# Kernel optimization log

Measured on AMD Instinct MI355X. Metric: run time of the kernel, lower is better.

The kernel has to match this reference:

```python
import jax, jax.numpy as jnp
import numpy as np

N_NODES = 50000
N_EDGES = 800000
N_PAIRS = 200000
IN_DIM = 128
HID = 64
OUT_DIM = 1


def _gat_layer(x, W, a_l, a_r, src, dst, n_nodes):
    # Single-head GAT (DGL-style): z = xW; attention logits from learned
    # left/right vectors; softmax over incoming edges of each dst node.
    z = x @ W                                   # [N, H]
    el = z @ a_l                                # [N]
    er = z @ a_r                                # [N]
    e = jax.nn.leaky_relu(el[src] + er[dst], 0.2)   # [E]
    emax = jax.ops.segment_max(e, dst, num_segments=n_nodes)  # [N]
    ex = jnp.exp(e - emax[dst])                 # [E], stable softmax numerator
    denom = jax.ops.segment_sum(ex, dst, num_segments=n_nodes)  # [N]
    msg = ex[:, None] * z[src]                  # [E, H]
    agg = jax.ops.segment_sum(msg, dst, num_segments=n_nodes)   # [N, H]
    return agg / jnp.maximum(denom, 1e-9)[:, None]


def setup_inputs() -> dict:
    key = jax.random.key(0)
    ks = jax.random.split(key, 10)
    feat = jax.random.normal(ks[0], (N_NODES, IN_DIM), dtype=jnp.float32)
    src = jax.random.randint(ks[1], (N_EDGES,), 0, N_NODES, dtype=jnp.int32)
    dst = jax.random.randint(ks[2], (N_EDGES,), 0, N_NODES, dtype=jnp.int32)
    # query pairs: take existing edges so the has_edges_between mask is true
    pair_src = src[:N_PAIRS]
    pair_dst = dst[:N_PAIRS]
    s1 = 1.0 / np.sqrt(IN_DIM)
    s2 = 1.0 / np.sqrt(HID)
    W1 = jax.random.normal(ks[3], (IN_DIM, HID), dtype=jnp.float32) * s1
    al1 = jax.random.normal(ks[4], (HID,), dtype=jnp.float32) * s2
    ar1 = jax.random.normal(ks[5], (HID,), dtype=jnp.float32) * s2
    W2 = jax.random.normal(ks[6], (HID, HID), dtype=jnp.float32) * s2
    al2 = jax.random.normal(ks[7], (HID,), dtype=jnp.float32) * s2
    ar2 = jax.random.normal(ks[8], (HID,), dtype=jnp.float32) * s2
    Wc = jax.random.normal(ks[9], (2 * HID, OUT_DIM), dtype=jnp.float32) * s2
    bc = jnp.zeros((OUT_DIM,), dtype=jnp.float32)
    return {"feat": feat, "W1": W1, "al1": al1, "ar1": ar1,
            "W2": W2, "al2": al2, "ar2": ar2, "Wc": Wc, "bc": bc,
            "src": src, "dst": dst, "pair_src": pair_src, "pair_dst": pair_dst}


def reference(feat, W1, al1, ar1, W2, al2, ar2, Wc, bc, src, dst, pair_src, pair_dst):
    src = src.astype(jnp.int32)
    dst = dst.astype(jnp.int32)
    # two hetero GAT layers (single ntype -> mean aggregate is identity) + ReLU
    h = jax.nn.relu(_gat_layer(feat, W1, al1, ar1, src, dst, N_NODES))
    h = jax.nn.relu(_gat_layer(h, W2, al2, ar2, src, dst, N_NODES))
    # has_edges_between(pair_src, pair_dst): membership test via sorted edge keys
    ekeys = src.astype(jnp.int64) * N_NODES + dst.astype(jnp.int64)
    skeys = jnp.sort(ekeys)
    pkeys = pair_src.astype(jnp.int64) * N_NODES + pair_dst.astype(jnp.int64)
    idx = jnp.clip(jnp.searchsorted(skeys, pkeys), 0, N_EDGES - 1)
    mask = (skeys[idx] == pkeys)                 # [P] bool
    # gather endpoint embeddings, concat, classify, sigmoid; invalid rows -> 0
    hs = h[pair_src]                             # [P, H]
    hd = h[pair_dst]                             # [P, H]
    h_pair = jnp.concatenate([hs, hd], axis=1)   # [P, 2H]
    out = jax.nn.sigmoid(h_pair @ Wc + bc)       # [P, OUT]
    return out * mask[:, None].astype(out.dtype)
```

## Files before the change

### kernel.cpp

```cpp
#include <hip/hip_runtime.h>
#include <cstdint>

#define N_NODES 50000
#define N_EDGES 800000
#define N_PAIRS 200000
#define IN_DIM 128
#define HID 64
#define N_WAVES_GEMM (N_NODES / 16)
#define NB1 196
#define CHUNK ((N_EDGES + NB1 - 1) / NB1)
#define MHIST (NB1 * NB1)
#define SBG ((MHIST + 255) / 256)
#define MB_GEMM ((N_WAVES_GEMM + 3) / 4)
#define NODE_BLOCKS ((N_NODES + 3) / 4)
#define MEMBER_BLOCKS (N_PAIRS / 32)

typedef __attribute__((ext_vector_type(8))) short bf16x8;
typedef __attribute__((ext_vector_type(4))) float f32x4;

__device__ __forceinline__ unsigned short bf16_rne(float f) {
    unsigned u = __float_as_uint(f);
    unsigned t = u + 0x7FFFu + ((u >> 16) & 1u);
    return (unsigned short)(t >> 16);
}
__device__ __forceinline__ void bf2f(unsigned u, float& a, float& b) {
    a = __uint_as_float(u << 16);
    b = __uint_as_float(u & 0xFFFF0000u);
}

__global__ __launch_bounds__(256) void hist_prep(
    const int* __restrict__ dst, int* __restrict__ histHi,
    const float* __restrict__ W1, const float* __restrict__ W2,
    unsigned short* __restrict__ w1hi, unsigned short* __restrict__ w1lo,
    unsigned short* __restrict__ w2hi, unsigned short* __restrict__ w2lo)
{
    const int t = threadIdx.x, b = blockIdx.x;
    if (b < NB1) {
        __shared__ int hist[256];
        hist[t] = 0; __syncthreads();
        const int beg = b * CHUNK, end = min(beg + CHUNK, N_EDGES);
        for (int e = beg + t; e < end; e += 256) atomicAdd(&hist[dst[e] >> 8], 1);
        __syncthreads();
        if (t < NB1) histHi[t * NB1 + b] = hist[t];
    } else {
        int tid = (b - NB1) * 256 + t;
        if (tid < 8192) {
            int jj = tid & 7, lane = (tid >> 3) & 63, tt = (tid >> 9) & 3, ks = tid >> 11;
            int k = ks * 32 + (lane >> 4) * 8 + jj;
            int n = tt * 16 + (lane & 15);
            float f = W1[k * HID + n];
            unsigned short hi = bf16_rne(f);
            float fhi = __uint_as_float(((unsigned)hi) << 16);
            w1hi[tid] = hi;
            w1lo[tid] = bf16_rne(f - fhi);
        }
        if (tid < 4096) {
            int jj = tid & 7, lane = (tid >> 3) & 63, tt = (tid >> 9) & 3, ks = tid >> 11;
            int k = ks * 32 + (lane >> 4) * 8 + jj;
            int n = tt * 16 + (lane & 15);
            float f = W2[k * HID + n];
            unsigned short hi = bf16_rne(f);
            float fhi = __uint_as_float(((unsigned)hi) << 16);
            w2hi[tid] = hi;
            w2lo[tid] = bf16_rne(f - fhi);
        }
    }
}

__global__ __launch_bounds__(256) void scan1g(
    int* __restrict__ histHi, int* __restrict__ bsums)
{
    __shared__ int sh[256];
    const int t = threadIdx.x;
    const int i = blockIdx.x * 256 + t;
    int v = (i < MHIST) ? histHi[i] : 0;
    sh[t] = v; __syncthreads();
    #pragma unroll
    for (int off = 1; off < 256; off <<= 1) {
        int x = sh[t];
        int a = (t >= off) ? sh[t - off] : 0;
        __syncthreads();
        sh[t] = x + a;
        __syncthreads();
    }
    if (i < MHIST) histHi[i] = sh[t] - v;
    if (t == 255) bsums[blockIdx.x] = sh[255];
}

__device__ __forceinline__ void scan_bsums(const int* __restrict__ bsums,
                                           int* sh, int* exb, int t)
{
    int v = (t < SBG) ? bsums[t] : 0;
    sh[t] = v; __syncthreads();
    #pragma unroll
    for (int off = 1; off < 256; off <<= 1) {
        int x = sh[t];
        int a = (t >= off) ? sh[t - off] : 0;
        __syncthreads();
        sh[t] = x + a;
        __syncthreads();
    }
    exb[t] = sh[t] - v;
    __syncthreads();
}

__device__ __forceinline__ void gemm1_body(
    int wave, int lane,
    const float* __restrict__ x,
    const unsigned short* __restrict__ whi, const unsigned short* __restrict__ wlo,
    const float* __restrict__ al, const float* __restrict__ ar,
    unsigned short* __restrict__ z, float* __restrict__ el, float* __restrict__ er)
{
    const int i0 = wave * 16;
    const int m = lane & 15, quad = lane >> 4;
    f32x4 acc[4] = {{0.f,0.f,0.f,0.f},{0.f,0.f,0.f,0.f},{0.f,0.f,0.f,0.f},{0.f,0.f,0.f,0.f}};
    const float* xrow = x + (size_t)(i0 + m) * IN_DIM;

    #pragma unroll 1
    for (int ks = 0; ks < 4; ++ks) {
        const float4 xv0 = *(const float4*)&xrow[ks * 32 + quad * 8];
        const float4 xv1 = *(const float4*)&xrow[ks * 32 + quad * 8 + 4];
        float xs[8] = {xv0.x, xv0.y, xv0.z, xv0.w, xv1.x, xv1.y, xv1.z, xv1.w};
        bf16x8 ahi, alo;
        #pragma unroll
        for (int jj = 0; jj < 8; ++jj) {
            unsigned short hb = bf16_rne(xs[jj]);
            float fhi = __uint_as_float(((unsigned)hb) << 16);
            ahi[jj] = (short)hb;
            alo[jj] = (short)bf16_rne(xs[jj] - fhi);
        }
        #pragma unroll
        for (int t = 0; t < 4; ++t) {
            const bf16x8 bhi = *(const bf16x8*)&whi[(((ks * 4 + t) * 64) + lane) * 8];
            const bf16x8 blo = *(const bf16x8*)&wlo[(((ks * 4 + t) * 64) + lane) * 8];
            acc[t] = __builtin_amdgcn_mfma_f32_16x16x32_bf16(ahi, bhi, acc[t], 0, 0, 0);
            acc[t] = __builtin_amdgcn_mfma_f32_16x16x32_bf16(ahi, blo, acc[t], 0, 0, 0);
            acc[t] = __builtin_amdgcn_mfma_f32_16x16x32_bf16(alo, bhi, acc[t], 0, 0, 0);
        }
    }
    #pragma unroll
    for (int r = 0; r < 4; ++r) {
        const int row = quad * 4 + r;
        float se = 0.f, sr = 0.f;
        #pragma unroll
        for (int t = 0; t < 4; ++t) {
            float v = acc[t][r];
            z[(size_t)(i0 + row) * HID + t * 16 + m] = bf16_rne(v);
            se = fmaf(v, al[t * 16 + m], se);
            sr = fmaf(v, ar[t * 16 + m], sr);
        }
        #pragma unroll
        for (int off = 1; off < 16; off <<= 1) {
            se += __shfl_xor(se, off, 64);
            sr += __shfl_xor(sr, off, 64);
        }
        if (m == 0) { el[i0 + row] = se; er[i0 + row] = sr; }
    }
}

__global__ __launch_bounds__(256) void scatter_gemm1(
    const int* __restrict__ src, const int* __restrict__ dst,
    const int* __restrict__ histEx, const int* __restrict__ bsums,
    unsigned* __restrict__ pairs,
    const float* __restrict__ x,
    const unsigned short* __restrict__ whi, const unsigned short* __restrict__ wlo,
    const float* __restrict__ al, const float* __restrict__ ar,
    unsigned short* __restrict__ z, float* __restrict__ el, float* __restrict__ er)
{
    const int b = blockIdx.x;
    if (b < NB1) {
        __shared__ int sh[256], exb[256], base[256];
        const int t = threadIdx.y * 64 + threadIdx.x;
        scan_bsums(bsums, sh, exb, t);
        if (t < NB1) {
            int idx = t * NB1 + b;
            base[t] = histEx[idx] + exb[idx >> 8];
        }
        __syncthreads();
        const int beg = b * CHUNK, end = min(beg + CHUNK, N_EDGES);
        for (int e = beg + t; e < end; e += 256) {
            int s = src[e], d = dst[e];
            int pos = atomicAdd(&base[d >> 8], 1);
            pairs[pos] = ((unsigned)s << 16) | (unsigned)d;
        }
    } else {
        const int wave = (b - NB1) * 4 + threadIdx.y;
        if (wave < N_WAVES_GEMM)
            gemm1_body(wave, threadIdx.x, x, whi, wlo, al, ar, z, el, er);
    }
}

__global__ __launch_bounds__(256) void seg_sort(
    const unsigned* __restrict__ pairs, const int* __restrict__ histEx,
    const int* __restrict__ bsums,
    int* __restrict__ row_start, unsigned short* __restrict__ csr_src)
{
    __shared__ int sh[256], exb[256], hist[256], sc[256], offs[256];
    const int t = threadIdx.x, b = blockIdx.x;
    scan_bsums(bsums, sh, exb, t);
    const int i0 = b * NB1;
    const int segStart = histEx[i0] + exb[i0 >> 8];
    int segEnd = N_EDGES;
    if (b < NB1 - 1) {
        const int i1 = (b + 1) * NB1;
        segEnd = histEx[i1] + exb[i1 >> 8];
    }
    hist[t] = 0; __syncthreads();
    for (int i = segStart + t; i < segEnd; i += 256)
        atomicAdd(&hist[pairs[i] & 255], 1);
    __syncthreads();
    int v = hist[t]; sc[t] = v; __syncthreads();
    #pragma unroll
    for (int off = 1; off < 256; off <<= 1) {
        int x = sc[t];
        int a = (t >= off) ? sc[t - off] : 0;
        __syncthreads();
        sc[t] = x + a;
        __syncthreads();
    }
    const int excl = sc[t] - v;
    offs[t] = segStart + excl;
    const int node = b * 256 + t;
    if (node <= N_NODES) row_start[node] = segStart + excl;
    __syncthreads();
    for (int i = segStart + t; i < segEnd; i += 256) {
        unsigned p = pairs[i];
        int pos = atomicAdd(&offs[p & 255], 1);
        csr_src[pos] = (unsigned short)(p >> 16);
    }
}

template <bool LAST>
__device__ __forceinline__ void agg_body(
    int i, int lane,
    const int* __restrict__ row_start, const unsigned short* __restrict__ csr_src,
    const float* __restrict__ el, const float* __restrict__ er,
    const unsigned short* __restrict__ z, unsigned short* __restrict__ h,
    const float* __restrict__ Wc, float* __restrict__ as, float* __restrict__ ad)
{
    const int rb = row_start[i], re = row_start[i + 1];
    const float er_i = er[i];
    const int es = lane >> 3;
    const int fl = lane & 7;

    float acc[8] = {0.f,0.f,0.f,0.f,0.f,0.f,0.f,0.f};
    float den = 0.f;

    int eA = rb + es;        bool vA = eA < re;
    int eB = eA + 8;         bool vB = eB < re;
    int sA = vA ? (int)csr_src[eA] : 0;
    int sB = vB ? (int)csr_src[eB] : 0;
    float elA = el[sA];
    uint4 zA = ((const uint4*)(z + (size_t)sA * HID))[fl];

    for (int e0 = rb; e0 < re; e0 += 8) {
        const int eC = e0 + 16 + es;
        const bool vC = eC < re;
        const int sC = vC ? (int)csr_src[eC] : 0;
        const float elB = el[sB];
        const uint4 zB = ((const uint4*)(z + (size_t)sB * HID))[fl];

        float x = elA + er_i;
        float lr = x > 0.f ? x : 0.2f * x;
        float ex = vA ? __expf(lr) : 0.f;
        float z0, z1, z2, z3, z4, z5, z6, z7;
        bf2f(zA.x, z0, z1); bf2f(zA.y, z2, z3);
        bf2f(zA.z, z4, z5); bf2f(zA.w, z6, z7);
        acc[0] = fmaf(ex, z0, acc[0]); acc[1] = fmaf(ex, z1, acc[1]);
        acc[2] = fmaf(ex, z2, acc[2]); acc[3] = fmaf(ex, z3, acc[3]);
        acc[4] = fmaf(ex, z4, acc[4]); acc[5] = fmaf(ex, z5, acc[5]);
        acc[6] = fmaf(ex, z6, acc[6]); acc[7] = fmaf(ex, z7, acc[7]);
        den += ex;

        sA = sB; vA = vB; elA = elB; zA = zB;
        sB = sC; vB = vC;
    }
    #pragma unroll
    for (int off = 8; off < 64; off <<= 1) {
        #pragma unroll
        for (int q = 0; q < 8; ++q) acc[q] += __shfl_xor(acc[q], off, 64);
        den += __shfl_xor(den, off, 64);
    }
    if (es == 0) {
        float inv = 1.f / fmaxf(den, 1e-9f);
        float hv[8];
        #pragma unroll
        for (int q = 0; q < 8; ++q) hv[q] = fmaxf(acc[q] * inv, 0.f);
        if (LAST) {
            float ps = 0.f, pd = 0.f;
            #pragma unroll
            for (int q = 0; q < 8; ++q) {
                ps = fmaf(hv[q], Wc[fl * 8 + q], ps);
                pd = fmaf(hv[q], Wc[HID + fl * 8 + q], pd);
            }
            #pragma unroll
            for (int off = 1; off < 8; off <<= 1) {
                ps += __shfl_xor(ps, off, 64);
                pd += __shfl_xor(pd, off, 64);
            }
            if (fl == 0) { as[i] = ps; ad[i] = pd; }
        } else {
            unsigned short o[8];
            #pragma unroll
            for (int q = 0; q < 8; ++q) o[q] = bf16_rne(hv[q]);
            uint4 pk;
            pk.x = (unsigned)o[0] | ((unsigned)o[1] << 16);
            pk.y = (unsigned)o[2] | ((unsigned)o[3] << 16);
            pk.z = (unsigned)o[4] | ((unsigned)o[5] << 16);
            pk.w = (unsigned)o[6] | ((unsigned)o[7] << 16);
            ((uint4*)(h + (size_t)i * HID))[fl] = pk;
        }
    }
}

__global__ __launch_bounds__(256) void agg1(
    const int* __restrict__ row_start, const unsigned short* __restrict__ csr_src,
    const float* __restrict__ el, const float* __restrict__ er,
    const unsigned short* __restrict__ z, unsigned short* __restrict__ h)
{
    const int i = blockIdx.x * 4 + threadIdx.y;
    if (i < N_NODES)
        agg_body<false>(i, threadIdx.x, row_start, csr_src, el, er, z, h,
                        nullptr, nullptr, nullptr);
}

__global__ __launch_bounds__(256) void gemm2_member(
    const unsigned short* __restrict__ x,
    const unsigned short* __restrict__ whi, const unsigned short* __restrict__ wlo,
    const float* __restrict__ al, const float* __restrict__ ar,
    unsigned short* __restrict__ z, float* __restrict__ el, float* __restrict__ er,
    const int* __restrict__ row_start, const unsigned short* __restrict__ csr_src,
    const int* __restrict__ ps, const int* __restrict__ pd, int* __restrict__ found)
{
    const int lane = threadIdx.x, b = blockIdx.x;
    if (b < MB_GEMM) {
        const int wave = b * 4 + threadIdx.y;
        if (wave >= N_WAVES_GEMM) return;
        const int i0 = wave * 16;
        const int m = lane & 15, quad = lane >> 4;
        f32x4 acc[4] = {{0.f,0.f,0.f,0.f},{0.f,0.f,0.f,0.f},{0.f,0.f,0.f,0.f},{0.f,0.f,0.f,0.f}};
        const unsigned short* xrow = x + (size_t)(i0 + m) * HID;
        #pragma unroll 1
        for (int ks = 0; ks < 2; ++ks) {
            const bf16x8 a = *(const bf16x8*)&xrow[ks * 32 + quad * 8];
            #pragma unroll
            for (int t = 0; t < 4; ++t) {
                const bf16x8 bhi = *(const bf16x8*)&whi[(((ks * 4 + t) * 64) + lane) * 8];
                const bf16x8 blo = *(const bf16x8*)&wlo[(((ks * 4 + t) * 64) + lane) * 8];
                acc[t] = __builtin_amdgcn_mfma_f32_16x16x32_bf16(a, bhi, acc[t], 0, 0, 0);
                acc[t] = __builtin_amdgcn_mfma_f32_16x16x32_bf16(a, blo, acc[t], 0, 0, 0);
            }
        }
        #pragma unroll
        for (int r = 0; r < 4; ++r) {
            const int row = quad * 4 + r;
            float se = 0.f, sr = 0.f;
            #pragma unroll
            for (int t = 0; t < 4; ++t) {
                float v = acc[t][r];
                z[(size_t)(i0 + row) * HID + t * 16 + m] = bf16_rne(v);
                se = fmaf(v, al[t * 16 + m], se);
                sr = fmaf(v, ar[t * 16 + m], sr);
            }
            #pragma unroll
            for (int off = 1; off < 16; off <<= 1) {
                se += __shfl_xor(se, off, 64);
                sr += __shfl_xor(sr, off, 64);
            }
            if (m == 0) { el[i0 + row] = se; er[i0 + row] = sr; }
        }
    } else {
        const int r = lane & 7, g = lane >> 3;
        const int p = (b - MB_GEMM) * 32 + threadIdx.y * 8 + g;
        const int s = ps[p], d = pd[p];
        const int rb = row_start[d], re = row_start[d + 1];
        int f = 0;
        for (int e = rb + r; e < re; e += 8) f |= ((int)csr_src[e] == s) ? 1 : 0;
        #pragma unroll
        for (int off = 1; off < 8; off <<= 1) f |= __shfl_xor(f, off, 64);
        if (r == 0) found[p] = f;
    }
}

__global__ __launch_bounds__(256) void agg2(
    const int* __restrict__ row_start, const unsigned short* __restrict__ csr_src,
    const float* __restrict__ el, const float* __restrict__ er,
    const unsigned short* __restrict__ z, const float* __restrict__ Wc,
    float* __restrict__ as, float* __restrict__ ad)
{
    const int i = blockIdx.x * 4 + threadIdx.y;
    if (i < N_NODES)
        agg_body<true>(i, threadIdx.x, row_start, csr_src, el, er, z,
                       nullptr, Wc, as, ad);
}

__global__ __launch_bounds__(256) void pair_tiny(
    const int* __restrict__ ps, const int* __restrict__ pd,
    const float* __restrict__ as, const float* __restrict__ ad,
    const float* __restrict__ bc, const int* __restrict__ found,
    float* __restrict__ out)
{
    const int p = blockIdx.x * 256 + threadIdx.x;
    if (p >= N_PAIRS) return;
    float v = as[ps[p]] + ad[pd[p]] + bc[0];
    float sg = 1.f / (1.f + __expf(-v));
    out[p] = found[p] ? sg : 0.f;
}

extern "C" void kernel_launch(void* const* d_in, const int* in_sizes, int n_in,
                              void* d_out, int out_size, void* d_ws, size_t ws_size,
                              hipStream_t stream)
{
    const float* feat = (const float*)d_in[0];
    const float* W1   = (const float*)d_in[1];
    const float* al1  = (const float*)d_in[2];
    const float* ar1  = (const float*)d_in[3];
    const float* W2   = (const float*)d_in[4];
    const float* al2  = (const float*)d_in[5];
    const float* ar2  = (const float*)d_in[6];
    const float* Wc   = (const float*)d_in[7];
    const float* bc   = (const float*)d_in[8];
    const int* src    = (const int*)d_in[9];
    const int* dst    = (const int*)d_in[10];
    const int* psrc   = (const int*)d_in[11];
    const int* pdst   = (const int*)d_in[12];
    float* out = (float*)d_out;

    char* ws = (char*)d_ws;
    unsigned short* z  = (unsigned short*)ws;  ws += (size_t)N_NODES * HID * 2;
    unsigned short* h1 = (unsigned short*)ws;  ws += (size_t)N_NODES * HID * 2;
    float* el = (float*)ws;               ws += (size_t)N_NODES * 4;
    float* er = (float*)ws;               ws += (size_t)N_NODES * 4;
    float* as = (float*)ws;               ws += (size_t)N_NODES * 4;
    float* ad = (float*)ws;               ws += (size_t)N_NODES * 4;
    int* row_start = (int*)ws;            ws += (size_t)(N_NODES + 1) * 4;
    int* histHi = (int*)ws;               ws += (size_t)MHIST * 4;
    int* bsumsA = (int*)ws;               ws += (size_t)(SBG + 1) * 4;
    int* found = (int*)ws;                ws += (size_t)N_PAIRS * 4;
    ws = (char*)(((uintptr_t)ws + 255) & ~(uintptr_t)255);
    unsigned* pairs = (unsigned*)ws;      ws += (size_t)N_EDGES * 4;
    unsigned short* csr_src = (unsigned short*)ws;  ws += (size_t)N_EDGES * 2;
    ws = (char*)(((uintptr_t)ws + 255) & ~(uintptr_t)255);
    unsigned short* w1hi = (unsigned short*)ws;  ws += 8192 * 2;
    unsigned short* w1lo = (unsigned short*)ws;  ws += 8192 * 2;
    unsigned short* w2hi = (unsigned short*)ws;  ws += 4096 * 2;
    unsigned short* w2lo = (unsigned short*)ws;  ws += 4096 * 2;

    dim3 b64x4(64, 4);

    hist_prep<<<NB1 + 32, 256, 0, stream>>>(dst, histHi, W1, W2, w1hi, w1lo, w2hi, w2lo);
    scan1g<<<SBG, 256, 0, stream>>>(histHi, bsumsA);
    scatter_gemm1<<<NB1 + MB_GEMM, b64x4, 0, stream>>>(src, dst, histHi, bsumsA, pairs,
        feat, w1hi, w1lo, al1, ar1, z, el, er);
    seg_sort<<<NB1, 256, 0, stream>>>(pairs, histHi, bsumsA, row_start, csr_src);
    agg1<<<NODE_BLOCKS, b64x4, 0, stream>>>(row_start, csr_src, el, er, z, h1);
    gemm2_member<<<MB_GEMM + MEMBER_BLOCKS, b64x4, 0, stream>>>(h1, w2hi, w2lo,
        al2, ar2, z, el, er, row_start, csr_src, psrc, pdst, found);
    agg2<<<NODE_BLOCKS, b64x4, 0, stream>>>(row_start, csr_src, el, er, z, Wc, as, ad);
    pair_tiny<<<(N_PAIRS + 255) / 256, 256, 0, stream>>>(psrc, pdst, as, ad, bc, found, out);
}
```

Before: 195.7 us.

## Merge preprocessing into cooperative kernel and fuse agg1 with layer-2 GEMM

Replaces the four preprocessing launches (histogram, scan, scatter+GEMM1, segment sort) with one cooperative persistent kernel that uses grid-wide syncs between phases. If the cooperative launch fails, it falls back to the old separate launches. It also fuses layer-1 aggregation with the layer-2 GEMM: each 16-node tile is aggregated into shared memory and multiplied there, so the h1 round trip through global memory and one launch go away. The cost is that grid-sync phases run with limited block counts, only one wave per block does the MFMA work, and the cooperative launch adds overhead.

```diff
diff --git a/kernel.cpp b/kernel.cpp
--- a/kernel.cpp
+++ b/kernel.cpp
@@ -1,5 +1,8 @@
 #include <hip/hip_runtime.h>
+#include <hip/hip_cooperative_groups.h>
 #include <cstdint>
+
+namespace cg = cooperative_groups;
 
 #define N_NODES 50000
 #define N_EDGES 800000
@@ -14,6 +17,8 @@
 #define MB_GEMM ((N_WAVES_GEMM + 3) / 4)
 #define NODE_BLOCKS ((N_NODES + 3) / 4)
 #define MEMBER_BLOCKS (N_PAIRS / 32)
+#define PRE_P0 (NB1 + 32)
+#define PRE_P2 (NB1 + MB_GEMM)
 
 typedef __attribute__((ext_vector_type(8))) short bf16x8;
 typedef __attribute__((ext_vector_type(4))) float f32x4;
@@ -28,51 +33,48 @@
     b = __uint_as_float(u & 0xFFFF0000u);
 }
 
-__global__ __launch_bounds__(256) void hist_prep(
-    const int* __restrict__ dst, int* __restrict__ histHi,
+
+__device__ __forceinline__ void hist_task(int b, int t,
+    const int* __restrict__ dst, int* __restrict__ histHi, int* hist)
+{
+    hist[t] = 0; __syncthreads();
+    const int beg = b * CHUNK, end = min(beg + CHUNK, N_EDGES);
+    for (int e = beg + t; e < end; e += 256) atomicAdd(&hist[dst[e] >> 8], 1);
+    __syncthreads();
+    if (t < NB1) histHi[t * NB1 + b] = hist[t];
+}
+
+__device__ __forceinline__ void wprep_task(int tid,
     const float* __restrict__ W1, const float* __restrict__ W2,
     unsigned short* __restrict__ w1hi, unsigned short* __restrict__ w1lo,
     unsigned short* __restrict__ w2hi, unsigned short* __restrict__ w2lo)
 {
-    const int t = threadIdx.x, b = blockIdx.x;
-    if (b < NB1) {
-        __shared__ int hist[256];
-        hist[t] = 0; __syncthreads();
-        const int beg = b * CHUNK, end = min(beg + CHUNK, N_EDGES);
-        for (int e = beg + t; e < end; e += 256) atomicAdd(&hist[dst[e] >> 8], 1);
-        __syncthreads();
-        if (t < NB1) histHi[t * NB1 + b] = hist[t];
-    } else {
-        int tid = (b - NB1) * 256 + t;
-        if (tid < 8192) {
-            int jj = tid & 7, lane = (tid >> 3) & 63, tt = (tid >> 9) & 3, ks = tid >> 11;
-            int k = ks * 32 + (lane >> 4) * 8 + jj;
-            int n = tt * 16 + (lane & 15);
-            float f = W1[k * HID + n];
-            unsigned short hi = bf16_rne(f);
-            float fhi = __uint_as_float(((unsigned)hi) << 16);
-            w1hi[tid] = hi;
-            w1lo[tid] = bf16_rne(f - fhi);
-        }
-        if (tid < 4096) {
-            int jj = tid & 7, lane = (tid >> 3) & 63, tt = (tid >> 9) & 3, ks = tid >> 11;
-            int k = ks * 32 + (lane >> 4) * 8 + jj;
-            int n = tt * 16 + (lane & 15);
-            float f = W2[k * HID + n];
-            unsigned short hi = bf16_rne(f);
-            float fhi = __uint_as_float(((unsigned)hi) << 16);
-            w2hi[tid] = hi;
-            w2lo[tid] = bf16_rne(f - fhi);
-        }
-    }
-}
-
-__global__ __launch_bounds__(256) void scan1g(
-    int* __restrict__ histHi, int* __restrict__ bsums)
-{
-    __shared__ int sh[256];
-    const int t = threadIdx.x;
-    const int i = blockIdx.x * 256 + t;
+    if (tid < 8192) {
+        int jj = tid & 7, lane = (tid >> 3) & 63, tt = (tid >> 9) & 3, ks = tid >> 11;
+        int k = ks * 32 + (lane >> 4) * 8 + jj;
+        int n = tt * 16 + (lane & 15);
+        float f = W1[k * HID + n];
+        unsigned short hi = bf16_rne(f);
+        float fhi = __uint_as_float(((unsigned)hi) << 16);
+        w1hi[tid] = hi;
+        w1lo[tid] = bf16_rne(f - fhi);
+    }
+    if (tid < 4096) {
+        int jj = tid & 7, lane = (tid >> 3) & 63, tt = (tid >> 9) & 3, ks = tid >> 11;
+        int k = ks * 32 + (lane >> 4) * 8 + jj;
+        int n = tt * 16 + (lane & 15);
+        float f = W2[k * HID + n];
+        unsigned short hi = bf16_rne(f);
+        float fhi = __uint_as_float(((unsigned)hi) << 16);
+        w2hi[tid] = hi;
+        w2lo[tid] = bf16_rne(f - fhi);
+    }
+}
+
+__device__ __forceinline__ void scan_task(int blk, int t,
+    int* __restrict__ histHi, int* __restrict__ bsums, int* sh)
+{
+    const int i = blk * 256 + t;
     int v = (i < MHIST) ? histHi[i] : 0;
     sh[t] = v; __syncthreads();
     #pragma unroll
@@ -84,7 +86,7 @@
         __syncthreads();
     }
     if (i < MHIST) histHi[i] = sh[t] - v;
-    if (t == 255) bsums[blockIdx.x] = sh[255];
+    if (t == 255) bsums[blk] = sh[255];
 }
 
 __device__ __forceinline__ void scan_bsums(const int* __restrict__ bsums,
@@ -104,6 +106,25 @@
     __syncthreads();
 }
 
+__device__ __forceinline__ void scatter_task(int b, int t,
+    const int* __restrict__ src, const int* __restrict__ dst,
+    const int* __restrict__ histEx, const int* __restrict__ bsums,
+    unsigned* __restrict__ pairs, int* sh, int* exb, int* base)
+{
+    scan_bsums(bsums, sh, exb, t);
+    if (t < NB1) {
+        int idx = t * NB1 + b;
+        base[t] = histEx[idx] + exb[idx >> 8];
+    }
+    __syncthreads();
+    const int beg = b * CHUNK, end = min(beg + CHUNK, N_EDGES);
+    for (int e = beg + t; e < end; e += 256) {
+        int s = src[e], d = dst[e];
+        int pos = atomicAdd(&base[d >> 8], 1);
+        pairs[pos] = ((unsigned)s << 16) | (unsigned)d;
+    }
+}
+
 __device__ __forceinline__ void gemm1_body(
     int wave, int lane,
     const float* __restrict__ x,
@@ -158,45 +179,12 @@
     }
 }
 
-__global__ __launch_bounds__(256) void scatter_gemm1(
-    const int* __restrict__ src, const int* __restrict__ dst,
-    const int* __restrict__ histEx, const int* __restrict__ bsums,
-    unsigned* __restrict__ pairs,
-    const float* __restrict__ x,
-    const unsigned short* __restrict__ whi, const unsigned short* __restrict__ wlo,
-    const float* __restrict__ al, const float* __restrict__ ar,
-    unsigned short* __restrict__ z, float* __restrict__ el, float* __restrict__ er)
-{
-    const int b = blockIdx.x;
-    if (b < NB1) {
-        __shared__ int sh[256], exb[256], base[256];
-        const int t = threadIdx.y * 64 + threadIdx.x;
-        scan_bsums(bsums, sh, exb, t);
-        if (t < NB1) {
-            int idx = t * NB1 + b;
-            base[t] = histEx[idx] + exb[idx >> 8];
-        }
-        __syncthreads();
-        const int beg = b * CHUNK, end = min(beg + CHUNK, N_EDGES);
-        for (int e = beg + t; e < end; e += 256) {
-            int s = src[e], d = dst[e];
-            int pos = atomicAdd(&base[d >> 8], 1);
-            pairs[pos] = ((unsigned)s << 16) | (unsigned)d;
-        }
-    } else {
-        const int wave = (b - NB1) * 4 + threadIdx.y;
-        if (wave < N_WAVES_GEMM)
-            gemm1_body(wave, threadIdx.x, x, whi, wlo, al, ar, z, el, er);
-    }
-}
-
-__global__ __launch_bounds__(256) void seg_sort(
+__device__ __forceinline__ void seg_sort_task(int b, int t,
     const unsigned* __restrict__ pairs, const int* __restrict__ histEx,
     const int* __restrict__ bsums,
-    int* __restrict__ row_start, unsigned short* __restrict__ csr_src)
-{
-    __shared__ int sh[256], exb[256], hist[256], sc[256], offs[256];
-    const int t = threadIdx.x, b = blockIdx.x;
+    int* __restrict__ row_start, unsigned short* __restrict__ csr_src,
+    int* sh, int* exb, int* hist, int* sc, int* offs)
+{
     scan_bsums(bsums, sh, exb, t);
     const int i0 = b * NB1;
     const int segStart = histEx[i0] + exb[i0 >> 8];
@@ -235,7 +223,7 @@
     int i, int lane,
     const int* __restrict__ row_start, const unsigned short* __restrict__ csr_src,
     const float* __restrict__ el, const float* __restrict__ er,
-    const unsigned short* __restrict__ z, unsigned short* __restrict__ h,
+    const unsigned short* __restrict__ z, unsigned short* __restrict__ hdst,
     const float* __restrict__ Wc, float* __restrict__ as, float* __restrict__ ad)
 {
     const int rb = row_start[i], re = row_start[i + 1];
@@ -308,77 +296,180 @@
             pk.y = (unsigned)o[2] | ((unsigned)o[3] << 16);
             pk.z = (unsigned)o[4] | ((unsigned)o[5] << 16);
             pk.w = (unsigned)o[6] | ((unsigned)o[7] << 16);
-            ((uint4*)(h + (size_t)i * HID))[fl] = pk;
-        }
-    }
-}
-
-__global__ __launch_bounds__(256) void agg1(
-    const int* __restrict__ row_start, const unsigned short* __restrict__ csr_src,
-    const float* __restrict__ el, const float* __restrict__ er,
-    const unsigned short* __restrict__ z, unsigned short* __restrict__ h)
-{
-    const int i = blockIdx.x * 4 + threadIdx.y;
-    if (i < N_NODES)
-        agg_body<false>(i, threadIdx.x, row_start, csr_src, el, er, z, h,
-                        nullptr, nullptr, nullptr);
-}
-
-__global__ __launch_bounds__(256) void gemm2_member(
-    const unsigned short* __restrict__ x,
+            ((uint4*)hdst)[fl] = pk;
+        }
+    }
+}
+
+
+__global__ __launch_bounds__(256) void hist_prep(
+    const int* __restrict__ dst, int* __restrict__ histHi,
+    const float* __restrict__ W1, const float* __restrict__ W2,
+    unsigned short* __restrict__ w1hi, unsigned short* __restrict__ w1lo,
+    unsigned short* __restrict__ w2hi, unsigned short* __restrict__ w2lo)
+{
+    __shared__ int hist[256];
+    const int t = threadIdx.x, b = blockIdx.x;
+    if (b < NB1) hist_task(b, t, dst, histHi, hist);
+    else wprep_task((b - NB1) * 256 + t, W1, W2, w1hi, w1lo, w2hi, w2lo);
+}
+
+__global__ __launch_bounds__(256) void scan1g(
+    int* __restrict__ histHi, int* __restrict__ bsums)
+{
+    __shared__ int sh[256];
+    scan_task(blockIdx.x, threadIdx.x, histHi, bsums, sh);
+}
+
+__global__ __launch_bounds__(256) void scatter_gemm1(
+    const int* __restrict__ src, const int* __restrict__ dst,
+    const int* __restrict__ histEx, const int* __restrict__ bsums,
+    unsigned* __restrict__ pairs,
+    const float* __restrict__ x,
     const unsigned short* __restrict__ whi, const unsigned short* __restrict__ wlo,
     const float* __restrict__ al, const float* __restrict__ ar,
-    unsigned short* __restrict__ z, float* __restrict__ el, float* __restrict__ er,
+    unsigned short* __restrict__ z, float* __restrict__ el, float* __restrict__ er)
+{
+    const int b = blockIdx.x;
+    if (b < NB1) {
+        __shared__ int sh[256], exb[256], base[256];
+        const int t = threadIdx.y * 64 + threadIdx.x;
+        scatter_task(b, t, src, dst, histEx, bsums, pairs, sh, exb, base);
+    } else {
+        const int wave = (b - NB1) * 4 + threadIdx.y;
+        if (wave < N_WAVES_GEMM)
+            gemm1_body(wave, threadIdx.x, x, whi, wlo, al, ar, z, el, er);
+    }
+}
+
+__global__ __launch_bounds__(256) void seg_sort(
+    const unsigned* __restrict__ pairs, const int* __restrict__ histEx,
+    const int* __restrict__ bsums,
+    int* __restrict__ row_start, unsigned short* __restrict__ csr_src)
+{
+    __shared__ int sh[256], exb[256], hist[256], sc[256], offs[256];
+    seg_sort_task(blockIdx.x, threadIdx.x, pairs, histEx, bsums,
+                  row_start, csr_src, sh, exb, hist, sc, offs);
+}
+
+struct PreArgs {
+    const int* src; const int* dst;
+    int* histHi; int* bsums;
+    unsigned* pairs;
+    const float* feat;
+    const float* W1; const float* W2;
+    unsigned short* w1hi; unsigned short* w1lo;
+    unsigned short* w2hi; unsigned short* w2lo;
+    const float* al1; const float* ar1;
+    unsigned short* z; float* el; float* er;
+    int* row_start; unsigned short* csr_src;
+};
+
+__global__ __launch_bounds__(256) void coop_pre(PreArgs a)
+{
+    __shared__ int sA[256], sB[256], sC[256], sD[256], sE[256];
+    cg::grid_group grid = cg::this_grid();
+    const int t = threadIdx.y * 64 + threadIdx.x;
+    const int G = (int)gridDim.x;
+
+    for (int task = blockIdx.x; task < PRE_P0; task += G) {
+        if (task < NB1) hist_task(task, t, a.dst, a.histHi, sA);
+        else wprep_task((task - NB1) * 256 + t, a.W1, a.W2, a.w1hi, a.w1lo, a.w2hi, a.w2lo);
+        __syncthreads();
+    }
+    grid.sync();
+
+    for (int task = blockIdx.x; task < SBG; task += G) {
+        scan_task(task, t, a.histHi, a.bsums, sA);
+        __syncthreads();
+    }
+    grid.sync();
+
+    for (int task = blockIdx.x; task < PRE_P2; task += G) {
+        if (task < NB1) {
+            scatter_task(task, t, a.src, a.dst, a.histHi, a.bsums, a.pairs, sA, sB, sC);
+        } else {
+            const int wave = (task - NB1) * 4 + threadIdx.y;
+            if (wave < N_WAVES_GEMM)
+                gemm1_body(wave, threadIdx.x, a.feat, a.w1hi, a.w1lo,
+                           a.al1, a.ar1, a.z, a.el, a.er);
+        }
+        __syncthreads();
+    }
+    grid.sync();
+
+    for (int task = blockIdx.x; task < NB1; task += G) {
+        seg_sort_task(task, t, a.pairs, a.histHi, a.bsums,
+                      a.row_start, a.csr_src, sA, sB, sC, sD, sE);
+        __syncthreads();
+    }
+}
+
+__global__ __launch_bounds__(256) void agg1_gemm2_member(
     const int* __restrict__ row_start, const unsigned short* __restrict__ csr_src,
+    const float* __restrict__ el1, const float* __restrict__ er1,
+    const unsigned short* __restrict__ z1,
+    const unsigned short* __restrict__ whi, const unsigned short* __restrict__ wlo,
+    const float* __restrict__ al, const float* __restrict__ ar,
+    unsigned short* __restrict__ z2, float* __restrict__ el2, float* __restrict__ er2,
     const int* __restrict__ ps, const int* __restrict__ pd, int* __restrict__ found)
 {
-    const int lane = threadIdx.x, b = blockIdx.x;
-    if (b < MB_GEMM) {
-        const int wave = b * 4 + threadIdx.y;
-        if (wave >= N_WAVES_GEMM) return;
-        const int i0 = wave * 16;
-        const int m = lane & 15, quad = lane >> 4;
-        f32x4 acc[4] = {{0.f,0.f,0.f,0.f},{0.f,0.f,0.f,0.f},{0.f,0.f,0.f,0.f},{0.f,0.f,0.f,0.f}};
-        const unsigned short* xrow = x + (size_t)(i0 + m) * HID;
+    const int b = blockIdx.x, lane = threadIdx.x, ty = threadIdx.y;
+    if (b < N_WAVES_GEMM) {
+        __shared__ __align__(16) unsigned short ht[16][72];
+        const int i0 = b * 16;
         #pragma unroll 1
-        for (int ks = 0; ks < 2; ++ks) {
-            const bf16x8 a = *(const bf16x8*)&xrow[ks * 32 + quad * 8];
-            #pragma unroll
-            for (int t = 0; t < 4; ++t) {
-                const bf16x8 bhi = *(const bf16x8*)&whi[(((ks * 4 + t) * 64) + lane) * 8];
-                const bf16x8 blo = *(const bf16x8*)&wlo[(((ks * 4 + t) * 64) + lane) * 8];
-                acc[t] = __builtin_amdgcn_mfma_f32_16x16x32_bf16(a, bhi, acc[t], 0, 0, 0);
-                acc[t] = __builtin_amdgcn_mfma_f32_16x16x32_bf16(a, blo, acc[t], 0, 0, 0);
-            }
-        }
-        #pragma unroll
-        for (int r = 0; r < 4; ++r) {
-            const int row = quad * 4 + r;
-            float se = 0.f, sr = 0.f;
-            #pragma unroll
-            for (int t = 0; t < 4; ++t) {
-                float v = acc[t][r];
-                z[(size_t)(i0 + row) * HID + t * 16 + m] = bf16_rne(v);
-                se = fmaf(v, al[t * 16 + m], se);
-                sr = fmaf(v, ar[t * 16 + m], sr);
+        for (int c = 0; c < 4; ++c) {
+            const int r = ty * 4 + c;
+            agg_body<false>(i0 + r, lane, row_start, csr_src, el1, er1, z1,
+                            &ht[r][0], nullptr, nullptr, nullptr);
+        }
+        __syncthreads();
+        if (ty == 0) {
+            const int m = lane & 15, quad = lane >> 4;
+            f32x4 acc[4] = {{0.f,0.f,0.f,0.f},{0.f,0.f,0.f,0.f},
+                            {0.f,0.f,0.f,0.f},{0.f,0.f,0.f,0.f}};
+            const unsigned short* xrow = &ht[m][0];
+            #pragma unroll 1
+            for (int ks = 0; ks < 2; ++ks) {
+                const bf16x8 aa = *(const bf16x8*)&xrow[ks * 32 + quad * 8];
+                #pragma unroll
+                for (int tt = 0; tt < 4; ++tt) {
+                    const bf16x8 bhi = *(const bf16x8*)&whi[(((ks * 4 + tt) * 64) + lane) * 8];
+                    const bf16x8 blo = *(const bf16x8*)&wlo[(((ks * 4 + tt) * 64) + lane) * 8];
+                    acc[tt] = __builtin_amdgcn_mfma_f32_16x16x32_bf16(aa, bhi, acc[tt], 0, 0, 0);
+                    acc[tt] = __builtin_amdgcn_mfma_f32_16x16x32_bf16(aa, blo, acc[tt], 0, 0, 0);
+                }
             }
             #pragma unroll
-            for (int off = 1; off < 16; off <<= 1) {
-                se += __shfl_xor(se, off, 64);
-                sr += __shfl_xor(sr, off, 64);
+            for (int r = 0; r < 4; ++r) {
+                const int row = quad * 4 + r;
+                float se = 0.f, sr = 0.f;
+                #pragma unroll
+                for (int tt = 0; tt < 4; ++tt) {
+                    float v = acc[tt][r];
+                    z2[(size_t)(i0 + row) * HID + tt * 16 + m] = bf16_rne(v);
+                    se = fmaf(v, al[tt * 16 + m], se);
+                    sr = fmaf(v, ar[tt * 16 + m], sr);
+                }
+                #pragma unroll
+                for (int off = 1; off < 16; off <<= 1) {
+                    se += __shfl_xor(se, off, 64);
+                    sr += __shfl_xor(sr, off, 64);
+                }
+                if (m == 0) { el2[i0 + row] = se; er2[i0 + row] = sr; }
             }
-            if (m == 0) { el[i0 + row] = se; er[i0 + row] = sr; }
         }
     } else {
-        const int r = lane & 7, g = lane >> 3;
-        const int p = (b - MB_GEMM) * 32 + threadIdx.y * 8 + g;
+        const int r8 = lane & 7, g = lane >> 3;
+        const int p = (b - N_WAVES_GEMM) * 32 + ty * 8 + g;
         const int s = ps[p], d = pd[p];
         const int rb = row_start[d], re = row_start[d + 1];
         int f = 0;
-        for (int e = rb + r; e < re; e += 8) f |= ((int)csr_src[e] == s) ? 1 : 0;
+        for (int e = rb + r8; e < re; e += 8) f |= ((int)csr_src[e] == s) ? 1 : 0;
         #pragma unroll
         for (int off = 1; off < 8; off <<= 1) f |= __shfl_xor(f, off, 64);
-        if (r == 0) found[p] = f;
+        if (r8 == 0) found[p] = f;
     }
 }
 
@@ -428,11 +519,13 @@
 
     char* ws = (char*)d_ws;
     unsigned short* z  = (unsigned short*)ws;  ws += (size_t)N_NODES * HID * 2;
-    unsigned short* h1 = (unsigned short*)ws;  ws += (size_t)N_NODES * HID * 2;
+    unsigned short* z2 = (unsigned short*)ws;  ws += (size_t)N_NODES * HID * 2;
     float* el = (float*)ws;               ws += (size_t)N_NODES * 4;
     float* er = (float*)ws;               ws += (size_t)N_NODES * 4;
     float* as = (float*)ws;               ws += (size_t)N_NODES * 4;
     float* ad = (float*)ws;               ws += (size_t)N_NODES * 4;
+    float* el2 = (float*)ws;              ws += (size_t)N_NODES * 4;
+    float* er2 = (float*)ws;              ws += (size_t)N_NODES * 4;
     int* row_start = (int*)ws;            ws += (size_t)(N_NODES + 1) * 4;
     int* histHi = (int*)ws;               ws += (size_t)MHIST * 4;
     int* bsumsA = (int*)ws;               ws += (size_t)(SBG + 1) * 4;
@@ -448,14 +541,33 @@
 
     dim3 b64x4(64, 4);
 
-    hist_prep<<<NB1 + 32, 256, 0, stream>>>(dst, histHi, W1, W2, w1hi, w1lo, w2hi, w2lo);
-    scan1g<<<SBG, 256, 0, stream>>>(histHi, bsumsA);
-    scatter_gemm1<<<NB1 + MB_GEMM, b64x4, 0, stream>>>(src, dst, histHi, bsumsA, pairs,
-        feat, w1hi, w1lo, al1, ar1, z, el, er);
-    seg_sort<<<NB1, 256, 0, stream>>>(pairs, histHi, bsumsA, row_start, csr_src);
-    agg1<<<NODE_BLOCKS, b64x4, 0, stream>>>(row_start, csr_src, el, er, z, h1);
-    gemm2_member<<<MB_GEMM + MEMBER_BLOCKS, b64x4, 0, stream>>>(h1, w2hi, w2lo,
-        al2, ar2, z, el, er, row_start, csr_src, psrc, pdst, found);
-    agg2<<<NODE_BLOCKS, b64x4, 0, stream>>>(row_start, csr_src, el, er, z, Wc, as, ad);
+    PreArgs pa;
+    pa.src = src; pa.dst = dst; pa.histHi = histHi; pa.bsums = bsumsA; pa.pairs = pairs;
+    pa.feat = feat; pa.W1 = W1; pa.W2 = W2;
+    pa.w1hi = w1hi; pa.w1lo = w1lo; pa.w2hi = w2hi; pa.w2lo = w2lo;
+    pa.al1 = al1; pa.ar1 = ar1; pa.z = z; pa.el = el; pa.er = er;
+    pa.row_start = row_start; pa.csr_src = csr_src;
+
+    int nb = 0;
+    hipError_t qe = hipOccupancyMaxActiveBlocksPerMultiprocessor(&nb, coop_pre, 256, 0);
+    int G = (qe == hipSuccess && nb > 0) ? nb * 256 : 256;
+    if (G > PRE_P2) G = PRE_P2;
+    void* kp[1] = { (void*)&pa };
+    hipError_t ce = hipLaunchCooperativeKernel(
+        reinterpret_cast<const void*>(&coop_pre), dim3((unsigned)G), b64x4, kp, 0, stream);
+    if (ce != hipSuccess) {
+        hist_prep<<<NB1 + 32, 256, 0, stream>>>(dst, histHi, W1, W2, w1hi, w1lo, w2hi, w2lo);
+        scan1g<<<SBG, 256, 0, stream>>>(histHi, bsumsA);
+        scatter_gemm1<<<PRE_P2, b64x4, 0, stream>>>(src, dst, histHi, bsumsA, pairs,
+            feat, w1hi, w1lo, al1, ar1, z, el, er);
+        seg_sort<<<NB1, 256, 0, stream>>>(pairs, histHi, bsumsA, row_start, csr_src);
+    }
+
+    agg1_gemm2_member<<<N_WAVES_GEMM + MEMBER_BLOCKS, b64x4, 0, stream>>>(
+        row_start, csr_src, el, er, z, w2hi, w2lo, al2, ar2,
+        z2, el2, er2, psrc, pdst, found);
+
+    agg2<<<NODE_BLOCKS, b64x4, 0, stream>>>(row_start, csr_src, el2, er2, z2, Wc, as, ad);
+
     pair_tiny<<<(N_PAIRS + 255) / 256, 256, 0, stream>>>(psrc, pdst, as, ad, bc, found, out);
 }
```

Measured after the change: 387.0 us. +97.8%, slower.

## Fuse layer-1 aggregation with layer-2 GEMM through shared memory

Applied to the files above, without the earlier changes.

Merges the agg1 kernel into the gemm2/membership kernel. Each block aggregates 16 nodes into a shared-memory tile, and one wave then runs the MFMA projection on that tile, so the h1 intermediate never goes to global memory and one launch is removed. Layer-2 z/el/er now go to separate buffers because other blocks still read layer-1 z/el/er. The cost is that only one of four waves does the GEMM after a block barrier, which reduces parallelism in that phase.

```diff
diff --git a/kernel.cpp b/kernel.cpp
--- a/kernel.cpp
+++ b/kernel.cpp
@@ -235,7 +235,7 @@
     int i, int lane,
     const int* __restrict__ row_start, const unsigned short* __restrict__ csr_src,
     const float* __restrict__ el, const float* __restrict__ er,
-    const unsigned short* __restrict__ z, unsigned short* __restrict__ h,
+    const unsigned short* __restrict__ z, unsigned short* __restrict__ hdst,
     const float* __restrict__ Wc, float* __restrict__ as, float* __restrict__ ad)
 {
     const int rb = row_start[i], re = row_start[i + 1];
@@ -308,77 +308,76 @@
             pk.y = (unsigned)o[2] | ((unsigned)o[3] << 16);
             pk.z = (unsigned)o[4] | ((unsigned)o[5] << 16);
             pk.w = (unsigned)o[6] | ((unsigned)o[7] << 16);
-            ((uint4*)(h + (size_t)i * HID))[fl] = pk;
-        }
-    }
-}
-
-__global__ __launch_bounds__(256) void agg1(
+            ((uint4*)hdst)[fl] = pk;
+        }
+    }
+}
+
+__global__ __launch_bounds__(256) void agg1_gemm2_member(
     const int* __restrict__ row_start, const unsigned short* __restrict__ csr_src,
-    const float* __restrict__ el, const float* __restrict__ er,
-    const unsigned short* __restrict__ z, unsigned short* __restrict__ h)
-{
-    const int i = blockIdx.x * 4 + threadIdx.y;
-    if (i < N_NODES)
-        agg_body<false>(i, threadIdx.x, row_start, csr_src, el, er, z, h,
-                        nullptr, nullptr, nullptr);
-}
-
-__global__ __launch_bounds__(256) void gemm2_member(
-    const unsigned short* __restrict__ x,
+    const float* __restrict__ el1, const float* __restrict__ er1,
+    const unsigned short* __restrict__ z1,
     const unsigned short* __restrict__ whi, const unsigned short* __restrict__ wlo,
     const float* __restrict__ al, const float* __restrict__ ar,
-    unsigned short* __restrict__ z, float* __restrict__ el, float* __restrict__ er,
-    const int* __restrict__ row_start, const unsigned short* __restrict__ csr_src,
+    unsigned short* __restrict__ z2, float* __restrict__ el2, float* __restrict__ er2,
     const int* __restrict__ ps, const int* __restrict__ pd, int* __restrict__ found)
 {
-    const int lane = threadIdx.x, b = blockIdx.x;
-    if (b < MB_GEMM) {
-        const int wave = b * 4 + threadIdx.y;
-        if (wave >= N_WAVES_GEMM) return;
-        const int i0 = wave * 16;
-        const int m = lane & 15, quad = lane >> 4;
-        f32x4 acc[4] = {{0.f,0.f,0.f,0.f},{0.f,0.f,0.f,0.f},{0.f,0.f,0.f,0.f},{0.f,0.f,0.f,0.f}};
-        const unsigned short* xrow = x + (size_t)(i0 + m) * HID;
+    const int b = blockIdx.x, lane = threadIdx.x, ty = threadIdx.y;
+    if (b < N_WAVES_GEMM) {
+        __shared__ __align__(16) unsigned short ht[16][72];
+        const int i0 = b * 16;
         #pragma unroll 1
-        for (int ks = 0; ks < 2; ++ks) {
-            const bf16x8 a = *(const bf16x8*)&xrow[ks * 32 + quad * 8];
-            #pragma unroll
-            for (int t = 0; t < 4; ++t) {
-                const bf16x8 bhi = *(const bf16x8*)&whi[(((ks * 4 + t) * 64) + lane) * 8];
-                const bf16x8 blo = *(const bf16x8*)&wlo[(((ks * 4 + t) * 64) + lane) * 8];
-                acc[t] = __builtin_amdgcn_mfma_f32_16x16x32_bf16(a, bhi, acc[t], 0, 0, 0);
-                acc[t] = __builtin_amdgcn_mfma_f32_16x16x32_bf16(a, blo, acc[t], 0, 0, 0);
-            }
-        }
-        #pragma unroll
-        for (int r = 0; r < 4; ++r) {
-            const int row = quad * 4 + r;
-            float se = 0.f, sr = 0.f;
-            #pragma unroll
-            for (int t = 0; t < 4; ++t) {
-                float v = acc[t][r];
-                z[(size_t)(i0 + row) * HID + t * 16 + m] = bf16_rne(v);
-                se = fmaf(v, al[t * 16 + m], se);
-                sr = fmaf(v, ar[t * 16 + m], sr);
+        for (int c = 0; c < 4; ++c) {
+            const int r = ty * 4 + c;
+            agg_body<false>(i0 + r, lane, row_start, csr_src, el1, er1, z1,
+                            &ht[r][0], nullptr, nullptr, nullptr);
+        }
+        __syncthreads();
+        if (ty == 0) {
+            const int m = lane & 15, quad = lane >> 4;
+            f32x4 acc[4] = {{0.f,0.f,0.f,0.f},{0.f,0.f,0.f,0.f},
+                            {0.f,0.f,0.f,0.f},{0.f,0.f,0.f,0.f}};
+            const unsigned short* xrow = &ht[m][0];
+            #pragma unroll 1
+            for (int ks = 0; ks < 2; ++ks) {
+                const bf16x8 aa = *(const bf16x8*)&xrow[ks * 32 + quad * 8];
+                #pragma unroll
+                for (int tt = 0; tt < 4; ++tt) {
+                    const bf16x8 bhi = *(const bf16x8*)&whi[(((ks * 4 + tt) * 64) + lane) * 8];
+                    const bf16x8 blo = *(const bf16x8*)&wlo[(((ks * 4 + tt) * 64) + lane) * 8];
+                    acc[tt] = __builtin_amdgcn_mfma_f32_16x16x32_bf16(aa, bhi, acc[tt], 0, 0, 0);
+                    acc[tt] = __builtin_amdgcn_mfma_f32_16x16x32_bf16(aa, blo, acc[tt], 0, 0, 0);
+                }
             }
             #pragma unroll
-            for (int off = 1; off < 16; off <<= 1) {
-                se += __shfl_xor(se, off, 64);
-                sr += __shfl_xor(sr, off, 64);
+            for (int r = 0; r < 4; ++r) {
+                const int row = quad * 4 + r;
+                float se = 0.f, sr = 0.f;
+                #pragma unroll
+                for (int tt = 0; tt < 4; ++tt) {
+                    float v = acc[tt][r];
+                    z2[(size_t)(i0 + row) * HID + tt * 16 + m] = bf16_rne(v);
+                    se = fmaf(v, al[tt * 16 + m], se);
+                    sr = fmaf(v, ar[tt * 16 + m], sr);
+                }
+                #pragma unroll
+                for (int off = 1; off < 16; off <<= 1) {
+                    se += __shfl_xor(se, off, 64);
+                    sr += __shfl_xor(sr, off, 64);
+                }
+                if (m == 0) { el2[i0 + row] = se; er2[i0 + row] = sr; }
             }
-            if (m == 0) { el[i0 + row] = se; er[i0 + row] = sr; }
         }
     } else {
-        const int r = lane & 7, g = lane >> 3;
-        const int p = (b - MB_GEMM) * 32 + threadIdx.y * 8 + g;
+        const int r8 = lane & 7, g = lane >> 3;
+        const int p = (b - N_WAVES_GEMM) * 32 + ty * 8 + g;
         const int s = ps[p], d = pd[p];
         const int rb = row_start[d], re = row_start[d + 1];
         int f = 0;
-        for (int e = rb + r; e < re; e += 8) f |= ((int)csr_src[e] == s) ? 1 : 0;
+        for (int e = rb + r8; e < re; e += 8) f |= ((int)csr_src[e] == s) ? 1 : 0;
         #pragma unroll
         for (int off = 1; off < 8; off <<= 1) f |= __shfl_xor(f, off, 64);
-        if (r == 0) found[p] = f;
+        if (r8 == 0) found[p] = f;
     }
 }
 
@@ -428,11 +427,13 @@
 
     char* ws = (char*)d_ws;
     unsigned short* z  = (unsigned short*)ws;  ws += (size_t)N_NODES * HID * 2;
-    unsigned short* h1 = (unsigned short*)ws;  ws += (size_t)N_NODES * HID * 2;
+    unsigned short* z2 = (unsigned short*)ws;  ws += (size_t)N_NODES * HID * 2;
     float* el = (float*)ws;               ws += (size_t)N_NODES * 4;
     float* er = (float*)ws;               ws += (size_t)N_NODES * 4;
     float* as = (float*)ws;               ws += (size_t)N_NODES * 4;
     float* ad = (float*)ws;               ws += (size_t)N_NODES * 4;
+    float* el2 = (float*)ws;              ws += (size_t)N_NODES * 4;
+    float* er2 = (float*)ws;              ws += (size_t)N_NODES * 4;
     int* row_start = (int*)ws;            ws += (size_t)(N_NODES + 1) * 4;
     int* histHi = (int*)ws;               ws += (size_t)MHIST * 4;
     int* bsumsA = (int*)ws;               ws += (size_t)(SBG + 1) * 4;
@@ -453,9 +454,9 @@
     scatter_gemm1<<<NB1 + MB_GEMM, b64x4, 0, stream>>>(src, dst, histHi, bsumsA, pairs,
         feat, w1hi, w1lo, al1, ar1, z, el, er);
     seg_sort<<<NB1, 256, 0, stream>>>(pairs, histHi, bsumsA, row_start, csr_src);
-    agg1<<<NODE_BLOCKS, b64x4, 0, stream>>>(row_start, csr_src, el, er, z, h1);
-    gemm2_member<<<MB_GEMM + MEMBER_BLOCKS, b64x4, 0, stream>>>(h1, w2hi, w2lo,
-        al2, ar2, z, el, er, row_start, csr_src, psrc, pdst, found);
-    agg2<<<NODE_BLOCKS, b64x4, 0, stream>>>(row_start, csr_src, el, er, z, Wc, as, ad);
+    agg1_gemm2_member<<<N_WAVES_GEMM + MEMBER_BLOCKS, b64x4, 0, stream>>>(
+        row_start, csr_src, el, er, z, w2hi, w2lo, al2, ar2,
+        z2, el2, er2, psrc, pdst, found);
+    agg2<<<NODE_BLOCKS, b64x4, 0, stream>>>(row_start, csr_src, el2, er2, z2, Wc, as, ad);
     pair_tiny<<<(N_PAIRS + 255) / 256, 256, 0, stream>>>(psrc, pdst, as, ad, bc, found, out);
 }
```

After: 185.2 us. 5.4% less time.
